# Kernel optimization log

Hardware: AMD Instinct MI355X
Metric: run time of the kernel (lower is better)

## Reference

```python
import jax, jax.numpy as jnp
import numpy as np

N_NODES = 50000
N_EDGES = 800000
K_HOPS = 4
F_IN, F_HID, A_DIM = 6, 128, 3


def gcn_norm(edge_index, edge_weight, num_nodes):
    # TAGConv(normalize=True) uses gcn_norm WITHOUT added self-loops:
    # norm = D^{-1/2}[src] * w * D^{-1/2}[dst], deg computed at target (col).
    row, col = edge_index[0], edge_index[1]
    deg = jax.ops.segment_sum(edge_weight, col, num_segments=num_nodes)
    deg_inv_sqrt = jnp.where(deg > 0, jax.lax.rsqrt(deg), 0.0)
    return deg_inv_sqrt[row] * edge_weight * deg_inv_sqrt[col]


def tag_conv(x, edge_index, norm_w, W, b):
    # out = sum_{k=0..K} (A_hat^k x) @ W[k] + b ; W: [K+1, in, out]
    row, col = edge_index[0], edge_index[1]
    out = x @ W[0]
    xk = x
    for k in range(1, W.shape[0]):
        # one sparse propagation hop: gather at src, scale, scatter-add at dst
        xk = jax.ops.segment_sum(norm_w[:, None] * xk[row], col, num_segments=x.shape[0])
        out = out + xk @ W[k]
    return out + b


def setup_inputs() -> dict:
    key = jax.random.key(0)
    ks = jax.random.split(key, 5)
    x = jax.random.normal(ks[0], (N_NODES, F_IN), dtype=jnp.float32)
    edge_index = jax.random.randint(ks[1], (2, N_EDGES), 0, N_NODES, dtype=jnp.int32)
    edge_weight = jax.random.uniform(ks[2], (N_EDGES,), dtype=jnp.float32)
    s1 = float(1.0 / np.sqrt(F_IN))
    s2 = float(1.0 / np.sqrt(F_HID))
    W1 = jax.random.uniform(ks[3], (K_HOPS + 1, F_IN, F_HID), minval=-s1, maxval=s1, dtype=jnp.float32)
    b1 = jnp.zeros((F_HID,), jnp.float32)
    W2 = jax.random.uniform(ks[4], (K_HOPS + 1, F_HID, 2 * A_DIM), minval=-s2, maxval=s2, dtype=jnp.float32)
    b2 = jnp.zeros((2 * A_DIM,), jnp.float32)
    return {"x": x, "edge_index": edge_index, "edge_weight": edge_weight,
            "W1": W1, "b1": b1, "W2": W2, "b2": b2}


def reference(x, edge_index, edge_weight, W1, b1, W2, b2):
    norm_w = gcn_norm(edge_index, edge_weight, x.shape[0])
    h = jax.nn.relu(tag_conv(x, edge_index, norm_w, W1, b1))
    out = tag_conv(h, edge_index, norm_w, W2, b2)
    mu = jnp.tanh(out[..., :A_DIM])
    logvar = jnp.tanh(out[..., A_DIM:])
    sigma = jnp.exp(2.0 * logvar)
    return mu, sigma
```

## Files before the change

kernel.cpp:

```cpp
#include <hip/hip_runtime.h>

#define NN 50000
#define NE 800000
#define KH 4
#define FIN 6
#define FH 128
#define FO 6
#define ADIM 3
#define NN8 (NN * 8)
#define NBKT 196
#define EPB 2048
#define NPB 391
#define CAP 6144
#define ROWMASK 0xFFFFFu
#define NEPAD (NE + NBKT * 1024)
#define NCH 4
#define NDB 196

typedef unsigned int u32;
typedef _Float16 f16;
typedef f16 f16x8 __attribute__((ext_vector_type(8)));

struct __align__(8) Edge { u32 r; float w; };

__device__ __forceinline__ float h2f_bits(u32 hb) {
    union { unsigned short us; f16 h; } c; c.us = (unsigned short)hb; return (float)c.h;
}
__device__ __forceinline__ u32 f2h_bits(float f) {
    union { unsigned short us; f16 h; } c; c.h = (f16)f; return (u32)c.us;
}
__device__ __forceinline__ u32 pack2(float a, float b) {
    return f2h_bits(a) | (f2h_bits(b) << 16);
}

__global__ void bucket_hist(const int* __restrict__ col, u32* __restrict__ ghist) {
    __shared__ u32 h[NBKT];
    for (int t = threadIdx.x; t < NBKT; t += 256) h[t] = 0;
    __syncthreads();
    int base = blockIdx.x * EPB;
#pragma unroll
    for (int i = 0; i < EPB / 256; ++i) {
        int e = base + i * 256 + threadIdx.x;
        if (e < NE) atomicAdd(&h[((u32)col[e]) >> 8], 1u);
    }
    __syncthreads();
    for (int t = threadIdx.x; t < NBKT; t += 256)
        if (h[t]) atomicAdd(&ghist[t], h[t]);
}

__global__ void bucket_scan(const u32* __restrict__ ghist, u32* __restrict__ bbase,
                            u32* __restrict__ bcur) {
    __shared__ u32 sh[256];
    int t = threadIdx.x;
    u32 v = (t < NBKT) ? ghist[t] : 0;
    sh[t] = v;
    __syncthreads();
    for (int off = 1; off < 256; off <<= 1) {
        u32 u = (t >= off) ? sh[t - off] : 0;
        __syncthreads();
        sh[t] += u;
        __syncthreads();
    }
    if (t < NBKT) { bbase[t] = sh[t] - v; bcur[t] = sh[t] - v; }
    if (t == NBKT - 1) bbase[NBKT] = sh[t];
}

__global__ __launch_bounds__(256) void partition_kernel(
        const int* __restrict__ row, const int* __restrict__ col,
        const float* __restrict__ w, u32* __restrict__ bcur,
        Edge* __restrict__ etmp) {
    __shared__ u32 hcnt[NBKT];
    __shared__ u32 hloc[NBKT];
    __shared__ u32 hglb[NBKT];
    __shared__ u32 smeta[EPB];
    __shared__ float swt[EPB];
    __shared__ u32 sgid[EPB];
    __shared__ u32 sc[256];
    for (int t = threadIdx.x; t < NBKT; t += 256) hcnt[t] = 0;
    __syncthreads();
    int base = blockIdx.x * EPB;
    u32 m_[8]; float w_[8]; u32 b_[8]; u32 rk_[8]; int v_[8];
#pragma unroll
    for (int i = 0; i < 8; ++i) {
        int e = base + i * 256 + threadIdx.x;
        v_[i] = e < NE;
        if (v_[i]) {
            u32 c = (u32)col[e];
            u32 r = (u32)row[e];
            b_[i] = c >> 8;
            m_[i] = ((c & 255u) << 20) | r;
            w_[i] = w[e];
            rk_[i] = atomicAdd(&hcnt[b_[i]], 1u);
        }
    }
    __syncthreads();
    {
        int t = threadIdx.x;
        u32 v = (t < NBKT) ? hcnt[t] : 0;
        sc[t] = v;
        __syncthreads();
        for (int off = 1; off < 256; off <<= 1) {
            u32 u = (t >= off) ? sc[t - off] : 0;
            __syncthreads();
            sc[t] += u;
            __syncthreads();
        }
        if (t < NBKT) hloc[t] = sc[t] - v;
    }
    __syncthreads();
    for (int t = threadIdx.x; t < NBKT; t += 256)
        if (hcnt[t]) hglb[t] = atomicAdd(&bcur[t], hcnt[t]);
    __syncthreads();
#pragma unroll
    for (int i = 0; i < 8; ++i) if (v_[i]) {
        u32 slot = hloc[b_[i]] + rk_[i];
        smeta[slot] = m_[i];
        swt[slot] = w_[i];
        sgid[slot] = hglb[b_[i]] + rk_[i];
    }
    __syncthreads();
    int tot = NE - base; if (tot > EPB) tot = EPB;
    for (int s = threadIdx.x; s < tot; s += 256) {
        Edge ed; ed.r = smeta[s]; ed.w = swt[s];
        etmp[sgid[s]] = ed;
    }
}

__global__ __launch_bounds__(256) void bucket_csr(
        const u32* __restrict__ bbase, const Edge* __restrict__ etmp,
        u32* __restrict__ edges, int* __restrict__ offs, int* __restrict__ eoff,
        float* __restrict__ dinv) {
    int b = blockIdx.x;
    int t = threadIdx.x;
    u32 s = bbase[b], e = bbase[b + 1];
    int cnt = (int)(e - s);
    u32 rb = s + (u32)b * 1024u;
    int node0 = b << 8;
    int nloc = NN - node0; if (nloc > 256) nloc = 256;
    __shared__ u32 ncnt[256];
    __shared__ float nsum[256];
    __shared__ u32 ncur[256];
    __shared__ u32 sc[256];
    __shared__ u32 stage[CAP];
    ncnt[t] = 0; nsum[t] = 0.f;
    __syncthreads();
    for (int i = t; i < cnt; i += 256) {
        Edge ed = etmp[s + i];
        u32 cl = ed.r >> 20;
        atomicAdd(&ncnt[cl], 1u);
        atomicAdd(&nsum[cl], ed.w);
    }
    __syncthreads();
    u32 v = ncnt[t];
    u32 pv = (v + 3u) & ~3u;
    sc[t] = pv;
    __syncthreads();
    for (int off = 1; off < 256; off <<= 1) {
        u32 u = (t >= off) ? sc[t - off] : 0;
        __syncthreads();
        sc[t] += u;
        __syncthreads();
    }
    u32 excl = sc[t] - pv;
    u32 ptot = sc[255];
    ncur[t] = excl;
    if (t < nloc) {
        offs[node0 + t] = (int)(rb + excl);
        eoff[node0 + t] = (int)(rb + excl + pv);
        float d = nsum[t];
        dinv[node0 + t] = d > 0.f ? rsqrtf(d) : 0.f;
    }
    __syncthreads();
    for (int i = t; i < cnt; i += 256) {
        Edge ed = etmp[s + i];
        u32 cl = ed.r >> 20;
        u32 slot = atomicAdd(&ncur[cl], 1u);
        u32 pw = (ed.r & ROWMASK) | (f2h_bits(ed.w) << 16);
        if (slot < CAP) stage[slot] = pw;
        else edges[rb + slot] = pw;
    }
    if (t < nloc) {
        for (u32 slot = excl + v; slot < excl + pv; ++slot) {
            if (slot < CAP) stage[slot] = 0u;
            else edges[rb + slot] = 0u;
        }
    }
    __syncthreads();
    int lim = (int)(ptot < CAP ? ptot : CAP);
    for (int i = t; i < lim; i += 256) edges[rb + i] = stage[i];
}

__global__ void pad_x(const float* __restrict__ x, f16* __restrict__ xpad,
                      const float* __restrict__ W1, const float* __restrict__ W2,
                      float* __restrict__ W1T, float* __restrict__ W2T,
                      u32* __restrict__ ghist) {
    int t = blockIdx.x * blockDim.x + threadIdx.x;
    if (t < NBKT) ghist[t] = 0;
    if (t < 30 * FH) {
        int f = t / 30, i = t - f * 30;
        W1T[t] = W1[i * FH + f];
        int k = i / 6, a = i - k * 6;
        W2T[t] = W2[((size_t)k * FH + f) * FO + a];
    }
    if (t >= NN8) return;
    int n = t >> 3, c = t & 7;
    xpad[t] = (c < 6) ? (f16)x[n * 6 + c] : (f16)0.f;
}

__device__ __forceinline__ void gath(const f16* __restrict__ xp, u32 r, float w,
                                     float& a0, float& a1, float& a2,
                                     float& a3, float& a4, float& a5) {
    f16x8 v = *(const f16x8*)(xp + (size_t)r * 8);
    a0 += w * (float)v[0]; a1 += w * (float)v[1]; a2 += w * (float)v[2];
    a3 += w * (float)v[3]; a4 += w * (float)v[4]; a5 += w * (float)v[5];
}

#define HOP_HEAD \
    int t = blockIdx.x * blockDim.x + threadIdx.x; \
    int n = t >> 2, j = t & 3; \
    if (n >= NN) return; \
    int s = offs[n], e = eoff[n]; \
    float a0 = 0.f, a1 = 0.f, a2 = 0.f, a3 = 0.f, a4 = 0.f, a5 = 0.f;

#define HOP_REDUCE \
    _Pragma("unroll") \
    for (int d = 1; d < 4; d <<= 1) { \
        a0 += __shfl_xor(a0, d); a1 += __shfl_xor(a1, d); a2 += __shfl_xor(a2, d); \
        a3 += __shfl_xor(a3, d); a4 += __shfl_xor(a4, d); a5 += __shfl_xor(a5, d); \
    }

__global__ void hop4(const int* __restrict__ offs, const int* __restrict__ eoff,
                     const u32* __restrict__ edges,
                     const f16* __restrict__ xprev, const float* __restrict__ yadd,
                     f16* __restrict__ xnext) {
    HOP_HEAD
    for (int i = s + 4 * j; i < e; i += 16) {
        int4 q = *(const int4*)(edges + i);
        { u32 wd = (u32)q.x; gath(xprev, wd & 0xFFFFu, h2f_bits(wd >> 16), a0, a1, a2, a3, a4, a5); }
        { u32 wd = (u32)q.y; gath(xprev, wd & 0xFFFFu, h2f_bits(wd >> 16), a0, a1, a2, a3, a4, a5); }
        { u32 wd = (u32)q.z; gath(xprev, wd & 0xFFFFu, h2f_bits(wd >> 16), a0, a1, a2, a3, a4, a5); }
        { u32 wd = (u32)q.w; gath(xprev, wd & 0xFFFFu, h2f_bits(wd >> 16), a0, a1, a2, a3, a4, a5); }
    }
    HOP_REDUCE
    float v0 = j == 0 ? a0 : j == 1 ? a2 : j == 2 ? a4 : 0.f;
    float v1 = j == 0 ? a1 : j == 1 ? a3 : j == 2 ? a5 : 0.f;
    if (yadd && j < 3) {
        v0 += yadd[(size_t)n * 32 + 2 * j];
        v1 += yadd[(size_t)n * 32 + 2 * j + 1];
    }
    ((u32*)xnext)[(size_t)n * 4 + j] = pack2(v0, v1);
}

__global__ void hop4_norm(const int* __restrict__ offs, const int* __restrict__ eoff,
                          u32* __restrict__ edges,
                          const float* __restrict__ dinv, const f16* __restrict__ xpad,
                          f16* __restrict__ xnext) {
    HOP_HEAD
    float dn = dinv[n];
    for (int i = s + 4 * j; i < e; i += 16) {
        int4 q = *(const int4*)(edges + i);
        int4 nq;
        { u32 wd = (u32)q.x; u32 r = wd & 0xFFFFu; float wn = h2f_bits(wd >> 16) * dn * dinv[r];
          nq.x = (int)(r | (f2h_bits(wn) << 16)); gath(xpad, r, wn, a0, a1, a2, a3, a4, a5); }
        { u32 wd = (u32)q.y; u32 r = wd & 0xFFFFu; float wn = h2f_bits(wd >> 16) * dn * dinv[r];
          nq.y = (int)(r | (f2h_bits(wn) << 16)); gath(xpad, r, wn, a0, a1, a2, a3, a4, a5); }
        { u32 wd = (u32)q.z; u32 r = wd & 0xFFFFu; float wn = h2f_bits(wd >> 16) * dn * dinv[r];
          nq.z = (int)(r | (f2h_bits(wn) << 16)); gath(xpad, r, wn, a0, a1, a2, a3, a4, a5); }
        { u32 wd = (u32)q.w; u32 r = wd & 0xFFFFu; float wn = h2f_bits(wd >> 16) * dn * dinv[r];
          nq.w = (int)(r | (f2h_bits(wn) << 16)); gath(xpad, r, wn, a0, a1, a2, a3, a4, a5); }
        *(int4*)(edges + i) = nq;
    }
    HOP_REDUCE
    float v0 = j == 0 ? a0 : j == 1 ? a2 : j == 2 ? a4 : 0.f;
    float v1 = j == 0 ? a1 : j == 1 ? a3 : j == 2 ? a5 : 0.f;
    ((u32*)xnext)[(size_t)n * 4 + j] = pack2(v0, v1);
}

__global__ void hop4_final(const int* __restrict__ offs, const int* __restrict__ eoff,
                           const u32* __restrict__ edges,
                           const f16* __restrict__ xprev, const float* __restrict__ y0,
                           float* __restrict__ out) {
    HOP_HEAD
    for (int i = s + 4 * j; i < e; i += 16) {
        int4 q = *(const int4*)(edges + i);
        { u32 wd = (u32)q.x; gath(xprev, wd & 0xFFFFu, h2f_bits(wd >> 16), a0, a1, a2, a3, a4, a5); }
        { u32 wd = (u32)q.y; gath(xprev, wd & 0xFFFFu, h2f_bits(wd >> 16), a0, a1, a2, a3, a4, a5); }
        { u32 wd = (u32)q.z; gath(xprev, wd & 0xFFFFu, h2f_bits(wd >> 16), a0, a1, a2, a3, a4, a5); }
        { u32 wd = (u32)q.w; gath(xprev, wd & 0xFFFFu, h2f_bits(wd >> 16), a0, a1, a2, a3, a4, a5); }
    }
    HOP_REDUCE
    if (j < 3) {
        float mv = (j == 0 ? a0 : j == 1 ? a1 : a2) + y0[(size_t)n * 32 + j];
        float sv = (j == 0 ? a3 : j == 1 ? a4 : a5) + y0[(size_t)n * 32 + 3 + j];
        out[n * ADIM + j] = tanhf(mv);
        out[NN * ADIM + n * ADIM + j] = expf(2.f * tanhf(sv));
    }
}

__global__ __launch_bounds__(256) void fused_dense_kernel(
        const float* __restrict__ x, const f16* __restrict__ xs,
        const float* __restrict__ W1T, const float* __restrict__ b1,
        const float* __restrict__ W2T,
        float* __restrict__ pacc) {
    int bb = blockIdx.x;
    int c = bb & (NCH - 1);
    int n = (bb >> 2) * 256 + threadIdx.x;
    if (n >= NN) return;
    float in[30];
    {
        const float* xr = x + (size_t)n * 6;
        float2 v0 = *(const float2*)xr;
        float2 v1 = *(const float2*)(xr + 2);
        float2 v2 = *(const float2*)(xr + 4);
        in[0] = v0.x; in[1] = v0.y; in[2] = v1.x;
        in[3] = v1.y; in[4] = v2.x; in[5] = v2.y;
    }
#pragma unroll
    for (int k = 0; k < 4; ++k) {
        f16x8 v = *(const f16x8*)(xs + (size_t)k * NN8 + (size_t)n * 8);
#pragma unroll
        for (int cc = 0; cc < 6; ++cc) in[6 + k * 6 + cc] = (float)v[cc];
    }
    float acc[32];
#pragma unroll
    for (int o = 0; o < 32; ++o) acc[o] = 0.f;
    int f0 = c * (FH / NCH);
#pragma unroll 2
    for (int fi = 0; fi < FH / NCH; ++fi) {
        int f = f0 + fi;
        const float* w1c = W1T + f * 30;
        float h = b1[f];
#pragma unroll
        for (int i = 0; i < 30; ++i) h = fmaf(in[i], w1c[i], h);
        h = h > 0.f ? h : 0.f;
        const float* w2c = W2T + f * 30;
#pragma unroll
        for (int o = 0; o < 30; ++o) acc[o] = fmaf(h, w2c[o], acc[o]);
    }
    float* pr = pacc + ((size_t)c * NN + n) * 32;
#pragma unroll
    for (int o4 = 0; o4 < 8; ++o4)
        *(float4*)(pr + o4 * 4) = make_float4(acc[o4 * 4], acc[o4 * 4 + 1],
                                              acc[o4 * 4 + 2], acc[o4 * 4 + 3]);
}

__global__ void reduce_dense(const float* __restrict__ pacc, const float* __restrict__ b2,
                             float* __restrict__ ys, f16* __restrict__ y4h) {
    int n = blockIdx.x * 256 + threadIdx.x;
    if (n >= NN) return;
    float acc[32];
#pragma unroll
    for (int o = 0; o < 32; ++o) acc[o] = 0.f;
#pragma unroll
    for (int c = 0; c < NCH; ++c) {
        const float* pr = pacc + ((size_t)c * NN + n) * 32;
#pragma unroll
        for (int o4 = 0; o4 < 8; ++o4) {
            float4 v = *(const float4*)(pr + o4 * 4);
            acc[o4 * 4 + 0] += v.x; acc[o4 * 4 + 1] += v.y;
            acc[o4 * 4 + 2] += v.z; acc[o4 * 4 + 3] += v.w;
        }
    }
#pragma unroll
    for (int o = 0; o < 6; ++o) acc[o] += b2[o];
    float* yr = ys + (size_t)n * 32;
#pragma unroll
    for (int o4 = 0; o4 < 6; ++o4)
        *(float4*)(yr + o4 * 4) = make_float4(acc[o4 * 4], acc[o4 * 4 + 1],
                                              acc[o4 * 4 + 2], acc[o4 * 4 + 3]);
    u32* yh = (u32*)(y4h + (size_t)n * 8);
    yh[0] = pack2(acc[24], acc[25]);
    yh[1] = pack2(acc[26], acc[27]);
    yh[2] = pack2(acc[28], acc[29]);
}

extern "C" void kernel_launch(void* const* d_in, const int* in_sizes, int n_in,
                              void* d_out, int out_size, void* d_ws, size_t ws_size,
                              hipStream_t stream) {
    const float* x  = (const float*)d_in[0];
    const int*   ei = (const int*)d_in[1];
    const float* ew = (const float*)d_in[2];
    const float* W1 = (const float*)d_in[3];
    const float* b1 = (const float*)d_in[4];
    const float* W2 = (const float*)d_in[5];
    const float* b2 = (const float*)d_in[6];
    float* out = (float*)d_out;

    const int* row = ei;
    const int* col = ei + NE;

    f16*   xpad  = (f16*)d_ws;
    f16*   xs    = xpad + NN8;
    f16*   y4h   = xs + (size_t)KH * NN8;
    f16*   za    = y4h + NN8;
    f16*   zb    = za + NN8;
    float* ys    = (float*)(zb + NN8);
    float* pacc  = ys + (size_t)NN * 32;
    float* W1T   = pacc + (size_t)NCH * NN * 32;
    float* W2T   = W1T + 30 * FH;
    Edge*  etmp  = (Edge*)(W2T + 30 * FH);
    u32*   edges = (u32*)(etmp + NE);
    u32*   ghist = edges + NEPAD;
    u32*   bbase = ghist + NBKT;
    u32*   bcur  = bbase + NBKT + 1;
    int*   offs  = (int*)(bcur + NBKT);
    int*   eoff  = offs + NN;
    float* dinv  = (float*)(eoff + NN);

    const int B = 256;
    const int gHop = (NN * 4 + B - 1) / B;
    const int gPad = (NN8 + B - 1) / B;

    pad_x<<<gPad, B, 0, stream>>>(x, xpad, W1, W2, W1T, W2T, ghist);
    bucket_hist<<<NPB, B, 0, stream>>>(col, ghist);
    bucket_scan<<<1, B, 0, stream>>>(ghist, bbase, bcur);
    partition_kernel<<<NPB, B, 0, stream>>>(row, col, ew, bcur, etmp);
    bucket_csr<<<NBKT, B, 0, stream>>>(bbase, etmp, edges, offs, eoff, dinv);

    hop4_norm<<<gHop, B, 0, stream>>>(offs, eoff, edges, dinv, xpad, xs);
    for (int k = 2; k <= KH; ++k)
        hop4<<<gHop, B, 0, stream>>>(offs, eoff, edges,
                                     xs + (size_t)(k - 2) * NN8, nullptr,
                                     xs + (size_t)(k - 1) * NN8);

    fused_dense_kernel<<<NDB * NCH, B, 0, stream>>>(x, xs, W1T, b1, W2T, pacc);
    reduce_dense<<<NDB, B, 0, stream>>>(pacc, b2, ys, y4h);

    hop4<<<gHop, B, 0, stream>>>(offs, eoff, edges, y4h, ys + 18, za);
    hop4<<<gHop, B, 0, stream>>>(offs, eoff, edges, za, ys + 12, zb);
    hop4<<<gHop, B, 0, stream>>>(offs, eoff, edges, zb, ys + 6, za);
    hop4_final<<<gHop, B, 0, stream>>>(offs, eoff, edges, za, ys, out);
}
```

Measured before the change: 146.7 us.

## Fuse padding into histogram kernel and fold bucket scan into consumers

Merges the x padding and weight transpose into the bucket histogram kernel. It also drops the standalone single-block scan kernel by having each partition and CSR block recompute the 196-entry prefix scan redundantly. Zeroing of the histogram and cursor arrays moves to a memset. This cuts the preprocessing launches from five to three plus a memset, at the cost of redundant per-block scans and extra barriers.

```diff
diff --git a/kernel.cpp b/kernel.cpp
--- a/kernel.cpp
+++ b/kernel.cpp
@@ -33,7 +33,22 @@
     return f2h_bits(a) | (f2h_bits(b) << 16);
 }
 
-__global__ void bucket_hist(const int* __restrict__ col, u32* __restrict__ ghist) {
+__global__ void hist_pad(const int* __restrict__ col, u32* __restrict__ ghist,
+                         const float* __restrict__ x, f16* __restrict__ xpad,
+                         const float* __restrict__ W1, const float* __restrict__ W2,
+                         float* __restrict__ W1T, float* __restrict__ W2T) {
+    int gtid = blockIdx.x * 256 + threadIdx.x;
+    int gsz = gridDim.x * 256;
+    for (int i = gtid; i < 30 * FH; i += gsz) {
+        int f = i / 30, k6 = i - f * 30;
+        W1T[i] = W1[k6 * FH + f];
+        int k = k6 / 6, a = k6 - k * 6;
+        W2T[i] = W2[((size_t)k * FH + f) * FO + a];
+    }
+    for (int i = gtid; i < NN8; i += gsz) {
+        int n = i >> 3, c = i & 7;
+        xpad[i] = (c < 6) ? (f16)x[n * 6 + c] : (f16)0.f;
+    }
     __shared__ u32 h[NBKT];
     for (int t = threadIdx.x; t < NBKT; t += 256) h[t] = 0;
     __syncthreads();
@@ -48,41 +63,38 @@
         if (h[t]) atomicAdd(&ghist[t], h[t]);
 }
 
-__global__ void bucket_scan(const u32* __restrict__ ghist, u32* __restrict__ bbase,
-                            u32* __restrict__ bcur) {
-    __shared__ u32 sh[256];
-    int t = threadIdx.x;
-    u32 v = (t < NBKT) ? ghist[t] : 0;
-    sh[t] = v;
-    __syncthreads();
-    for (int off = 1; off < 256; off <<= 1) {
-        u32 u = (t >= off) ? sh[t - off] : 0;
-        __syncthreads();
-        sh[t] += u;
-        __syncthreads();
-    }
-    if (t < NBKT) { bbase[t] = sh[t] - v; bcur[t] = sh[t] - v; }
-    if (t == NBKT - 1) bbase[NBKT] = sh[t];
-}
-
 __global__ __launch_bounds__(256) void partition_kernel(
         const int* __restrict__ row, const int* __restrict__ col,
-        const float* __restrict__ w, u32* __restrict__ bcur,
-        Edge* __restrict__ etmp) {
+        const float* __restrict__ w, const u32* __restrict__ ghist,
+        u32* __restrict__ bcur0, Edge* __restrict__ etmp) {
     __shared__ u32 hcnt[NBKT];
     __shared__ u32 hloc[NBKT];
     __shared__ u32 hglb[NBKT];
+    __shared__ u32 hbase[NBKT];
     __shared__ u32 smeta[EPB];
     __shared__ float swt[EPB];
     __shared__ u32 sgid[EPB];
     __shared__ u32 sc[256];
-    for (int t = threadIdx.x; t < NBKT; t += 256) hcnt[t] = 0;
+    int t = threadIdx.x;
+    {
+        u32 v = (t < NBKT) ? ghist[t] : 0;
+        sc[t] = v;
+        __syncthreads();
+        for (int off = 1; off < 256; off <<= 1) {
+            u32 u = (t >= off) ? sc[t - off] : 0;
+            __syncthreads();
+            sc[t] += u;
+            __syncthreads();
+        }
+        if (t < NBKT) hbase[t] = sc[t] - v;
+    }
+    for (int i = t; i < NBKT; i += 256) hcnt[i] = 0;
     __syncthreads();
     int base = blockIdx.x * EPB;
     u32 m_[8]; float w_[8]; u32 b_[8]; u32 rk_[8]; int v_[8];
 #pragma unroll
     for (int i = 0; i < 8; ++i) {
-        int e = base + i * 256 + threadIdx.x;
+        int e = base + i * 256 + t;
         v_[i] = e < NE;
         if (v_[i]) {
             u32 c = (u32)col[e];
@@ -95,7 +107,6 @@
     }
     __syncthreads();
     {
-        int t = threadIdx.x;
         u32 v = (t < NBKT) ? hcnt[t] : 0;
         sc[t] = v;
         __syncthreads();
@@ -108,8 +119,8 @@
         if (t < NBKT) hloc[t] = sc[t] - v;
     }
     __syncthreads();
-    for (int t = threadIdx.x; t < NBKT; t += 256)
-        if (hcnt[t]) hglb[t] = atomicAdd(&bcur[t], hcnt[t]);
+    for (int i = t; i < NBKT; i += 256)
+        if (hcnt[i]) hglb[i] = hbase[i] + atomicAdd(&bcur0[i], hcnt[i]);
     __syncthreads();
 #pragma unroll
     for (int i = 0; i < 8; ++i) if (v_[i]) {
@@ -120,30 +131,43 @@
     }
     __syncthreads();
     int tot = NE - base; if (tot > EPB) tot = EPB;
-    for (int s = threadIdx.x; s < tot; s += 256) {
+    for (int s = t; s < tot; s += 256) {
         Edge ed; ed.r = smeta[s]; ed.w = swt[s];
         etmp[sgid[s]] = ed;
     }
 }
 
 __global__ __launch_bounds__(256) void bucket_csr(
-        const u32* __restrict__ bbase, const Edge* __restrict__ etmp,
+        const u32* __restrict__ ghist, const Edge* __restrict__ etmp,
         u32* __restrict__ edges, int* __restrict__ offs, int* __restrict__ eoff,
         float* __restrict__ dinv) {
     int b = blockIdx.x;
     int t = threadIdx.x;
-    u32 s = bbase[b], e = bbase[b + 1];
-    int cnt = (int)(e - s);
-    u32 rb = s + (u32)b * 1024u;
-    int node0 = b << 8;
-    int nloc = NN - node0; if (nloc > 256) nloc = 256;
     __shared__ u32 ncnt[256];
     __shared__ float nsum[256];
     __shared__ u32 ncur[256];
     __shared__ u32 sc[256];
     __shared__ u32 stage[CAP];
+    __shared__ u32 sbase[2];
     ncnt[t] = 0; nsum[t] = 0.f;
-    __syncthreads();
+    {
+        u32 v = (t < NBKT) ? ghist[t] : 0;
+        sc[t] = v;
+        __syncthreads();
+        for (int off = 1; off < 256; off <<= 1) {
+            u32 u = (t >= off) ? sc[t - off] : 0;
+            __syncthreads();
+            sc[t] += u;
+            __syncthreads();
+        }
+        if (t == b) { sbase[0] = sc[t] - v; sbase[1] = sc[t]; }
+        __syncthreads();
+    }
+    u32 s = sbase[0], e = sbase[1];
+    int cnt = (int)(e - s);
+    u32 rb = s + (u32)b * 1024u;
+    int node0 = b << 8;
+    int nloc = NN - node0; if (nloc > 256) nloc = 256;
     for (int i = t; i < cnt; i += 256) {
         Edge ed = etmp[s + i];
         u32 cl = ed.r >> 20;
@@ -188,23 +212,6 @@
     __syncthreads();
     int lim = (int)(ptot < CAP ? ptot : CAP);
     for (int i = t; i < lim; i += 256) edges[rb + i] = stage[i];
-}
-
-__global__ void pad_x(const float* __restrict__ x, f16* __restrict__ xpad,
-                      const float* __restrict__ W1, const float* __restrict__ W2,
-                      float* __restrict__ W1T, float* __restrict__ W2T,
-                      u32* __restrict__ ghist) {
-    int t = blockIdx.x * blockDim.x + threadIdx.x;
-    if (t < NBKT) ghist[t] = 0;
-    if (t < 30 * FH) {
-        int f = t / 30, i = t - f * 30;
-        W1T[t] = W1[i * FH + f];
-        int k = i / 6, a = i - k * 6;
-        W2T[t] = W2[((size_t)k * FH + f) * FO + a];
-    }
-    if (t >= NN8) return;
-    int n = t >> 3, c = t & 7;
-    xpad[t] = (c < 6) ? (f16)x[n * 6 + c] : (f16)0.f;
 }
 
 __device__ __forceinline__ void gath(const f16* __restrict__ xp, u32 r, float w,
@@ -401,21 +408,18 @@
     Edge*  etmp  = (Edge*)(W2T + 30 * FH);
     u32*   edges = (u32*)(etmp + NE);
     u32*   ghist = edges + NEPAD;
-    u32*   bbase = ghist + NBKT;
-    u32*   bcur  = bbase + NBKT + 1;
-    int*   offs  = (int*)(bcur + NBKT);
+    u32*   bcur0 = ghist + NBKT;
+    int*   offs  = (int*)(bcur0 + NBKT);
     int*   eoff  = offs + NN;
     float* dinv  = (float*)(eoff + NN);
 
     const int B = 256;
     const int gHop = (NN * 4 + B - 1) / B;
-    const int gPad = (NN8 + B - 1) / B;
-
-    pad_x<<<gPad, B, 0, stream>>>(x, xpad, W1, W2, W1T, W2T, ghist);
-    bucket_hist<<<NPB, B, 0, stream>>>(col, ghist);
-    bucket_scan<<<1, B, 0, stream>>>(ghist, bbase, bcur);
-    partition_kernel<<<NPB, B, 0, stream>>>(row, col, ew, bcur, etmp);
-    bucket_csr<<<NBKT, B, 0, stream>>>(bbase, etmp, edges, offs, eoff, dinv);
+
+    hipMemsetAsync(ghist, 0, 2 * NBKT * sizeof(u32), stream);
+    hist_pad<<<NPB, B, 0, stream>>>(col, ghist, x, xpad, W1, W2, W1T, W2T);
+    partition_kernel<<<NPB, B, 0, stream>>>(row, col, ew, ghist, bcur0, etmp);
+    bucket_csr<<<NBKT, B, 0, stream>>>(ghist, etmp, edges, offs, eoff, dinv);
 
     hop4_norm<<<gHop, B, 0, stream>>>(offs, eoff, edges, dinv, xpad, xs);
     for (int k = 2; k <= KH; ++k)
```

Result: no change. 147.3 us (+0.4%).
